# Performance work log

Measured on AMD Instinct MI355X. Metric: run time of the kernel, lower is better.

The kernel has to match this reference:

```python
import jax, jax.numpy as jnp
import numpy as np

N_VUL = 100000
N_OTH = 20000
E = 400000
IN_DIM = 256
OUT_DIM = 128
NTYPES = ['vul', 'weakness_name', 'product_name', 'refer', 'descr']
NSIZE = [N_VUL, N_OTH, N_OTH, N_OTH, N_OTH]
# canonical etypes as (src_ntype_idx, dst_ntype_idx), in loop order:
#   w2v, p2v (positive -> vul), r2v, d2v (negative -> vul), v2w, v2p, v2r, v2d (vul -> others)
CE = [(1, 0), (2, 0), (3, 0), (4, 0), (0, 1), (0, 2), (0, 3), (0, 4)]
EPS = 1e-8


def setup_inputs() -> dict:
    key = jax.random.key(0)
    ks = jax.random.split(key, 7)
    feat_vul = jax.random.normal(ks[0], (N_VUL, IN_DIM), jnp.float32)
    feat_other = jax.random.normal(ks[1], (4, N_OTH, IN_DIM), jnp.float32)
    We = jax.random.normal(ks[2], (8, IN_DIM, OUT_DIM), jnp.float32) * 0.05
    Wn = jax.random.normal(ks[3], (5, IN_DIM, OUT_DIM), jnp.float32) * 0.05
    bn = jax.random.normal(ks[4], (5, OUT_DIM), jnp.float32) * 0.05
    src = jax.random.randint(ks[5], (8, E), 0, 100000, jnp.int32)
    dst = jax.random.randint(ks[6], (8, E), 0, 100000, jnp.int32)
    src_idx = jnp.stack([src[i] % NSIZE[CE[i][0]] for i in range(8)])
    dst_idx = jnp.stack([dst[i] % NSIZE[CE[i][1]] for i in range(8)])
    return dict(feat_vul=feat_vul, feat_other=feat_other, We=We, Wn=Wn, bn=bn,
                src_idx=src_idx, dst_idx=dst_idx)


def _forward(feat_vul, feat_other, We, Wn, bn, src_idx, dst_idx):
    feats = [feat_vul] + [feat_other[i] for i in range(4)]
    # per-ntype dst projection ht (same nweight regardless of etype)
    ht = [feats[n] @ Wn[n] + bn[n] for n in range(5)]

    # apply_edges pass: scores use the per-etype hr projection (fresh at apply time);
    # hr is overwritten per etype, so messages later use the LAST hr written per src type.
    scores = []
    hr_final = [None] * 5
    for i, (s_t, d_t) in enumerate(CE):
        hr = feats[s_t] @ We[i]                     # [N_src, OUT]
        hr_final[s_t] = hr
        a = hr[src_idx[i]]                          # [E, OUT] gather
        b = ht[d_t][dst_idx[i]]                     # [E, OUT] gather
        dot = jnp.sum(a * b, axis=1)
        na = jnp.maximum(jnp.linalg.norm(a, axis=1), EPS)
        nb = jnp.maximum(jnp.linalg.norm(b, axis=1), EPS)
        scores.append(dot / (na * nb))              # cosine similarity [E]

    # multi_update_all: per-etype segment weighted-sum of messages + mean attention
    agg_h, ma = [], []
    for i, (s_t, d_t) in enumerate(CE):
        s = scores[i]
        m = s[:, None] * hr_final[s_t][src_idx[i]]  # [E, OUT]
        n_dst = NSIZE[d_t]
        h = jax.ops.segment_sum(m, dst_idx[i], num_segments=n_dst)
        cnt = jax.ops.segment_sum(jnp.ones_like(s), dst_idx[i], num_segments=n_dst)
        mean_s = jax.ops.segment_sum(s, dst_idx[i], num_segments=n_dst) / jnp.maximum(cnt, 1.0)
        agg_h.append(h)
        ma.append(mean_s)

    # vul (target): stack positive etypes (w2v,p2v) and negative (r2v,d2v) along dim 1
    ph = jnp.stack([agg_h[0], agg_h[1]], axis=1)            # [N_vul, 2, OUT]
    mpa = jnp.stack([ma[0], ma[1]], axis=1)[:, :, None]     # [N_vul, 2, 1]
    nh = jnp.stack([agg_h[2], agg_h[3]], axis=1)
    mna = jnp.stack([ma[2], ma[3]], axis=1)[:, :, None]
    pa = jax.nn.softmax(mpa, axis=1) * 0.6
    na_w = jax.nn.softmax(mna, axis=1) * 0.4
    h_vul = jnp.sum(pa * ph, axis=1) + jnp.sum(na_w * nh, axis=1)
    outs = [jnp.concatenate([ht[0], h_vul], axis=1)]

    # other ntypes: single-etype stack -> softmax over size-1 dim = 1.0
    for j, e in enumerate([4, 5, 6, 7]):
        n = j + 1
        hs = agg_h[e][:, None, :]                           # [N, 1, OUT]
        ms = ma[e][:, None, None]                           # [N, 1, 1]
        h = jnp.sum(jax.nn.softmax(ms, axis=1) * hs, axis=1)
        outs.append(jnp.concatenate([ht[n], h], axis=1))
    return tuple(outs)


def reference(feat_vul, feat_other, We, Wn, bn, src_idx, dst_idx):
    return _forward(feat_vul, feat_other, We, Wn, bn, src_idx, dst_idx)
```

## Files before the change

### kernel.cpp

```cpp
#include <hip/hip_runtime.h>

#define N_VUL 100000
#define N_OTH 20000
#define E_NUM 400000
#define K_DIM 256
#define D_OUT 128
#define EPS 1e-8f
#define LDW 264

#define NCV 391
#define NCO_J 79
#define NC (NCV + 4 * NCO_J)
#define TOT_E (8 * E_NUM)
#define CHUNK 8192
#define VCAP 5120
#define OCAP 6144
#define VKEYS (4 * N_VUL)
#define KEYS  (4 * N_VUL + 4 * N_OTH)

typedef __attribute__((ext_vector_type(8))) short bf16x8;
typedef __attribute__((ext_vector_type(4))) float f32x4;

static const size_t NV128 = (size_t)N_VUL * 128;
static const size_t NO128 = (size_t)N_OTH * 128;

__device__ __forceinline__ unsigned short f2b(float f) {
    unsigned int u = __float_as_uint(f);
    u += 0x7FFFu + ((u >> 16) & 1u);
    return (unsigned short)(u >> 16);
}
__device__ __forceinline__ float b2f(unsigned short h) {
    return __uint_as_float(((unsigned int)h) << 16);
}

__global__ __launch_bounds__(256)
void probe_idx(const int* __restrict__ cand, int* __restrict__ flag)
{
    const int e = blockIdx.x * 256 + threadIdx.x;
    if (e >= E_NUM) return;
    int v = cand[e];
    if (v < 0 || v >= N_OTH) atomicOr(flag, 1);
}

__global__ __launch_bounds__(256)
void pack_w(const float* __restrict__ We, const float* __restrict__ Wn,
            unsigned short* __restrict__ Wb)
{
    const int id = blockIdx.x * 256 + threadIdx.x;
    if (id >= 13 * 32768) return;
    const int wp = id >> 15;
    const int n  = (id >> 8) & 127;
    const int k  = id & 255;
    const float* S;
    if (wp == 0)      S = Wn;
    else if (wp <= 4) S = We + (size_t)(3 + wp) * 32768;
    else if (wp & 1)  S = Wn + (size_t)((wp - 3) >> 1) * 32768;
    else              S = We + (size_t)((wp - 6) >> 1) * 32768;
    Wb[id] = f2b(S[k * D_OUT + n]);
}

__global__ __launch_bounds__(256)
void proj_mfma(const float* __restrict__ X, const unsigned short* __restrict__ Wb,
               const float* __restrict__ bias, float* __restrict__ outF,
               unsigned short* __restrict__ tabs, int NW, int N)
{
    __shared__ unsigned short xs[64 * LDW];
    const int tid  = threadIdx.x;
    const int wave = tid >> 6, lane = tid & 63;
    const int r0   = blockIdx.x * 64;

    #pragma unroll
    for (int c = 0; c < 16; ++c) {
        int f = c * 256 + tid;
        int row = f >> 6, col4 = f & 63;
        int gr = r0 + row; if (gr >= N) gr = N - 1;
        float4 v = *(const float4*)(X + (size_t)gr * K_DIM + col4 * 4);
        unsigned short* p = xs + row * LDW + col4 * 4;
        p[0] = f2b(v.x); p[1] = f2b(v.y); p[2] = f2b(v.z); p[3] = f2b(v.w);
    }
    __syncthreads();

    const int n0   = wave * 32;
    const int arow = lane & 15, akd = (lane >> 4) * 8;
    const int bcol = lane & 15, bkd = (lane >> 4) * 8;
    const int rsub = (lane >> 4) * 4;

    float bias0 = 0.f, bias1 = 0.f;
    if (bias) { bias0 = bias[n0 + bcol]; bias1 = bias[n0 + 16 + bcol]; }

    for (int w = 0; w < NW; ++w) {
        f32x4 acc[4][2];
        #pragma unroll
        for (int m = 0; m < 4; ++m) {
            acc[m][0] = (f32x4){0.f, 0.f, 0.f, 0.f};
            acc[m][1] = (f32x4){0.f, 0.f, 0.f, 0.f};
        }
        const unsigned short* wb = Wb + (size_t)w * 128 * 256;
        #pragma unroll
        for (int k = 0; k < 8; ++k) {
            bf16x8 b0 = *(const bf16x8*)(wb + (size_t)(n0 + bcol) * 256 + k * 32 + bkd);
            bf16x8 b1 = *(const bf16x8*)(wb + (size_t)(n0 + 16 + bcol) * 256 + k * 32 + bkd);
            #pragma unroll
            for (int m = 0; m < 4; ++m) {
                bf16x8 a = *(const bf16x8*)(xs + (m * 16 + arow) * LDW + k * 32 + akd);
                acc[m][0] = __builtin_amdgcn_mfma_f32_16x16x32_bf16(a, b0, acc[m][0], 0, 0, 0);
                acc[m][1] = __builtin_amdgcn_mfma_f32_16x16x32_bf16(a, b1, acc[m][1], 0, 0, 0);
            }
        }
        if (w == 0) {
            #pragma unroll
            for (int m = 0; m < 4; ++m)
                #pragma unroll
                for (int nn = 0; nn < 2; ++nn) {
                    const int col = n0 + nn * 16 + bcol;
                    const float bb = nn ? bias1 : bias0;
                    #pragma unroll
                    for (int j = 0; j < 4; ++j) {
                        const int row = r0 + m * 16 + rsub + j;
                        if (row < N) outF[(size_t)row * 256 + col] = acc[m][nn][j] + bb;
                    }
                }
        } else {
            unsigned short* tw = tabs + (size_t)(w - 1) * N * D_OUT;
            #pragma unroll
            for (int m = 0; m < 4; ++m)
                #pragma unroll
                for (int nn = 0; nn < 2; ++nn) {
                    const int col = n0 + nn * 16 + bcol;
                    #pragma unroll
                    for (int j = 0; j < 4; ++j) {
                        const int row = r0 + m * 16 + rsub + j;
                        if (row < N) tw[(size_t)row * D_OUT + col] = f2b(acc[m][nn][j]);
                    }
                }
        }
    }
}

__global__ __launch_bounds__(256)
void rownorm_f(const float* __restrict__ T, float* __restrict__ rn, int N)
{
    const int lr = threadIdx.x >> 6;
    const int l  = threadIdx.x & 63;
    const int r  = blockIdx.x * 4 + lr;
    if (r >= N) return;
    float a = T[(size_t)r * 256 + l];
    float b = T[(size_t)r * 256 + 64 + l];
    float s = a * a + b * b;
    #pragma unroll
    for (int m = 32; m; m >>= 1) s += __shfl_xor(s, m);
    if (l == 0) rn[r] = 1.f / fmaxf(sqrtf(s), EPS);
}

__global__ __launch_bounds__(256)
void rownorm_b(const unsigned short* __restrict__ T, float* __restrict__ rn, int N)
{
    const int lr = threadIdx.x >> 6;
    const int l  = threadIdx.x & 63;
    const int r  = blockIdx.x * 4 + lr;
    if (r >= N) return;
    float a = b2f(T[(size_t)r * D_OUT + l]);
    float b = b2f(T[(size_t)r * D_OUT + 64 + l]);
    float s = a * a + b * b;
    #pragma unroll
    for (int m = 32; m; m >>= 1) s += __shfl_xor(s, m);
    if (l == 0) rn[r] = 1.f / fmaxf(sqrtf(s), EPS);
}

__device__ __forceinline__ void edge_cd(const int* __restrict__ srcp,
                                        const int* __restrict__ dstp,
                                        int id, int* c_out, unsigned* entry_out)
{
    const int et = id / E_NUM;
    const int e  = id - et * E_NUM;
    int d = dstp[(size_t)et * E_NUM + e];
    if (et < 4) {
        d = d < 0 ? 0 : (d >= N_VUL ? N_VUL - 1 : d);
        *c_out = d >> 8;
        if (entry_out) {
            int s = srcp[(size_t)et * E_NUM + e];
            s = s < 0 ? 0 : (s >= N_OTH ? N_OTH - 1 : s);
            *entry_out = ((unsigned)(((d & 255) << 2) | et) << 17) | (unsigned)s;
        }
    } else {
        d = d < 0 ? 0 : (d >= N_OTH ? N_OTH - 1 : d);
        *c_out = NCV + (et - 4) * NCO_J + (d >> 8);
        if (entry_out) {
            int s = srcp[(size_t)et * E_NUM + e];
            s = s < 0 ? 0 : (s >= N_VUL ? N_VUL - 1 : s);
            *entry_out = ((unsigned)(d & 255) << 17) | (unsigned)s;
        }
    }
}

__global__ __launch_bounds__(256)
void chist(const int* __restrict__ pA, const int* __restrict__ pB,
           const int* __restrict__ flag, int* __restrict__ ccnt)
{
    __shared__ int h[NC];
    for (int i = threadIdx.x; i < NC; i += 256) h[i] = 0;
    __syncthreads();
    const int flagv = *flag;
    const int* srcp = flagv ? pB : pA;
    const int* dstp = flagv ? pA : pB;
    const int base = blockIdx.x * 16384;
    for (int t = 0; t < 64; ++t) {
        const int id = base + t * 256 + threadIdx.x;
        if (id < TOT_E) {
            int c; edge_cd(srcp, dstp, id, &c, nullptr);
            atomicAdd(&h[c], 1);
        }
    }
    __syncthreads();
    for (int i = threadIdx.x; i < NC; i += 256)
        if (h[i]) atomicAdd(&ccnt[i], h[i]);
}

__global__ __launch_bounds__(256)
void cscan(const int* __restrict__ ccnt, int* __restrict__ cbase,
           int* __restrict__ ccur, int* __restrict__ offs)
{
    __shared__ int sh[256];
    __shared__ int carry;
    if (threadIdx.x == 0) carry = 0;
    __syncthreads();
    for (int b = 0; b < NC; b += 256) {
        const int i = b + threadIdx.x;
        const int v = (i < NC) ? ccnt[i] : 0;
        sh[threadIdx.x] = v;
        __syncthreads();
        for (int st = 1; st < 256; st <<= 1) {
            int t = (threadIdx.x >= st) ? sh[threadIdx.x - st] : 0;
            __syncthreads();
            sh[threadIdx.x] += t;
            __syncthreads();
        }
        const int excl = carry + sh[threadIdx.x] - v;
        if (i < NC) { cbase[i] = excl; ccur[i] = excl; }
        __syncthreads();
        if (threadIdx.x == 255) carry += sh[255];
        __syncthreads();
    }
    if (threadIdx.x == 0) offs[KEYS] = carry;
}

__global__ __launch_bounds__(256)
void cstage(const int* __restrict__ pA, const int* __restrict__ pB,
            const int* __restrict__ flag, int* __restrict__ ccur,
            unsigned* __restrict__ staging)
{
    __shared__ unsigned outE[CHUNK];
    __shared__ unsigned short binof[CHUNK];
    __shared__ int foff[NC];
    __shared__ int fcur[NC];
    __shared__ int gb[NC];
    __shared__ int sh[256];
    __shared__ int carry;

    const int flagv = *flag;
    const int* srcp = flagv ? pB : pA;
    const int* dstp = flagv ? pA : pB;
    const int base = blockIdx.x * CHUNK;
    const int n = (base + CHUNK <= TOT_E) ? CHUNK : (TOT_E - base);

    for (int i = threadIdx.x; i < NC; i += 256) foff[i] = 0;
    if (threadIdx.x == 0) carry = 0;
    __syncthreads();

    for (int t = 0; t < CHUNK / 256; ++t) {
        const int k = t * 256 + threadIdx.x;
        if (k < n) {
            int c; edge_cd(srcp, dstp, base + k, &c, nullptr);
            atomicAdd(&foff[c], 1);
        }
    }
    __syncthreads();

    for (int b = 0; b < NC; b += 256) {
        const int i = b + threadIdx.x;
        const int v = (i < NC) ? foff[i] : 0;
        sh[threadIdx.x] = v;
        __syncthreads();
        for (int st = 1; st < 256; st <<= 1) {
            int t = (threadIdx.x >= st) ? sh[threadIdx.x - st] : 0;
            __syncthreads();
            sh[threadIdx.x] += t;
            __syncthreads();
        }
        const int excl = carry + sh[threadIdx.x] - v;
        if (i < NC) {
            foff[i] = excl;
            fcur[i] = excl;
            gb[i] = v ? atomicAdd(&ccur[i], v) : 0;
        }
        __syncthreads();
        if (threadIdx.x == 255) carry += sh[255];
        __syncthreads();
    }

    for (int t = 0; t < CHUNK / 256; ++t) {
        const int k = t * 256 + threadIdx.x;
        if (k < n) {
            int c; unsigned ent;
            edge_cd(srcp, dstp, base + k, &c, &ent);
            const int p = atomicAdd(&fcur[c], 1);
            outE[p] = ent;
            binof[p] = (unsigned short)c;
        }
    }
    __syncthreads();

    for (int i = threadIdx.x; i < n; i += 256) {
        const int c = binof[i];
        staging[gb[c] + (i - foff[c])] = outE[i];
    }
}

__global__ __launch_bounds__(256)
void fine_sort_vul(const unsigned* __restrict__ staging,
                   const int* __restrict__ cbase, const int* __restrict__ ccnt,
                   int* __restrict__ srcs, int* __restrict__ offs)
{
    __shared__ unsigned raw[VCAP];
    __shared__ int srt[VCAP];
    __shared__ int foff[1025];
    __shared__ int fcur[1024];
    __shared__ int sh[256];
    __shared__ int carry;

    const int c = blockIdx.x;
    const int nb = min(ccnt[c], VCAP);
    const int gb = cbase[c];
    const int tid = threadIdx.x;

    for (int i = tid; i < 1024; i += 256) fcur[i] = 0;
    if (tid == 0) carry = 0;
    __syncthreads();
    for (int i = tid; i < nb; i += 256) {
        unsigned e = staging[gb + i];
        raw[i] = e;
        atomicAdd(&fcur[e >> 17], 1);
    }
    __syncthreads();
    for (int b = 0; b < 1024; b += 256) {
        const int i = b + tid;
        const int v = fcur[i];
        sh[tid] = v;
        __syncthreads();
        for (int st = 1; st < 256; st <<= 1) {
            int t = (tid >= st) ? sh[tid - st] : 0;
            __syncthreads();
            sh[tid] += t;
            __syncthreads();
        }
        foff[i] = carry + sh[tid] - v;
        __syncthreads();
        if (tid == 255) carry += sh[255];
        __syncthreads();
    }
    __syncthreads();
    for (int i = tid; i < 1024; i += 256) fcur[i] = foff[i];
    __syncthreads();
    for (int i = tid; i < nb; i += 256) {
        unsigned e = raw[i];
        const int p = atomicAdd(&fcur[e >> 17], 1);
        srt[p] = (int)(e & 0x1FFFFu);
    }
    __syncthreads();
    for (int i = tid; i < nb; i += 256) srcs[gb + i] = srt[i];
    for (int lk = tid; lk < 1024; lk += 256) {
        const int d = c * 256 + (lk >> 2);
        if (d < N_VUL) offs[c * 1024 + lk] = gb + foff[lk];
    }
}

__global__ __launch_bounds__(256)
void fine_sort_oth(const unsigned* __restrict__ staging,
                   const int* __restrict__ cbase, const int* __restrict__ ccnt,
                   int* __restrict__ srcs, int* __restrict__ offs)
{
    __shared__ unsigned raw[OCAP];
    __shared__ int srt[OCAP];
    __shared__ int foff[257];
    __shared__ int fcur[256];
    __shared__ int sh[256];

    const int co = blockIdx.x;
    const int j = co / NCO_J, dg = co - j * NCO_J;
    const int c = NCV + co;
    const int nb = min(ccnt[c], OCAP);
    const int gb = cbase[c];
    const int tid = threadIdx.x;

    fcur[tid] = 0;
    __syncthreads();
    for (int i = tid; i < nb; i += 256) {
        unsigned e = staging[gb + i];
        raw[i] = e;
        atomicAdd(&fcur[e >> 17], 1);
    }
    __syncthreads();
    {
        const int v = fcur[tid];
        sh[tid] = v;
        __syncthreads();
        for (int st = 1; st < 256; st <<= 1) {
            int t = (tid >= st) ? sh[tid - st] : 0;
            __syncthreads();
            sh[tid] += t;
            __syncthreads();
        }
        foff[tid] = sh[tid] - v;
        if (tid == 255) foff[256] = sh[255];
        __syncthreads();
        fcur[tid] = foff[tid];
    }
    __syncthreads();
    for (int i = tid; i < nb; i += 256) {
        unsigned e = raw[i];
        const int p = atomicAdd(&fcur[e >> 17], 1);
        srt[p] = (int)(e & 0x1FFFFu);
    }
    __syncthreads();
    for (int i = tid; i < nb; i += 256) srcs[gb + i] = srt[i];
    {
        const int d = dg * 256 + tid;
        if (d < N_OTH) offs[VKEYS + j * N_OTH + d] = gb + foff[tid];
    }
}

__global__ __launch_bounds__(256)
void vul_gather(const int* __restrict__ srcs, const int* __restrict__ offs,
                const unsigned short* __restrict__ othTab,
                const float* __restrict__ rinHrS,
                const float* __restrict__ rinHtVul,
                float* __restrict__ out)
{
    const int d = blockIdx.x * 4 + (threadIdx.x >> 6);
    const int lane = threadIdx.x & 63;
    const int g = lane >> 4, l = lane & 15;

    const float* hrow = out + (size_t)d * 256 + l * 8;
    float b0[8];
    {
        float4 t0 = *(const float4*)(hrow);
        float4 t1 = *(const float4*)(hrow + 4);
        b0[0] = t0.x; b0[1] = t0.y; b0[2] = t0.z; b0[3] = t0.w;
        b0[4] = t1.x; b0[5] = t1.y; b0[6] = t1.z; b0[7] = t1.w;
    }
    const float rnb = rinHtVul[d];

    float acc[4][8];
    float ss[4];
    #pragma unroll
    for (int et = 0; et < 4; ++et) {
        ss[et] = 0.f;
        #pragma unroll
        for (int j = 0; j < 8; ++j) acc[et][j] = 0.f;
    }

    #pragma unroll
    for (int et = 0; et < 4; ++et) {
        const unsigned short* T = othTab + (size_t)et * NO128;
        const float* rA = rinHrS + (size_t)et * N_OTH;
        const int k0 = offs[d * 4 + et], k1 = offs[d * 4 + et + 1];
        for (int p0 = k0; p0 < k1; p0 += 4) {
            const int p = p0 + g;
            const bool ok = (p < k1);
            const int s = srcs[ok ? p : k0];
            bf16x8 av = *(const bf16x8*)(T + (size_t)s * 128 + l * 8);
            float a[8];
            #pragma unroll
            for (int j = 0; j < 8; ++j) a[j] = b2f((unsigned short)av[j]);
            float dp = 0.f;
            #pragma unroll
            for (int j = 0; j < 8; ++j) dp = fmaf(a[j], b0[j], dp);
            dp += __shfl_xor(dp, 1); dp += __shfl_xor(dp, 2);
            dp += __shfl_xor(dp, 4); dp += __shfl_xor(dp, 8);
            const float v = ok ? dp * rA[s] * rnb : 0.f;
            ss[et] += v;
            #pragma unroll
            for (int j = 0; j < 8; ++j) acc[et][j] = fmaf(v, a[j], acc[et][j]);
        }
    }

    #pragma unroll
    for (int et = 0; et < 4; ++et) {
        float t = ss[et];
        t += __shfl_xor(t, 16); t += __shfl_xor(t, 32);
        ss[et] = t;
    }
    const int o0 = offs[d * 4], o1 = offs[d * 4 + 1], o2 = offs[d * 4 + 2],
              o3 = offs[d * 4 + 3], o4 = offs[d * 4 + 4];
    const float m0 = ss[0] / fmaxf((float)(o1 - o0), 1.f);
    const float m1 = ss[1] / fmaxf((float)(o2 - o1), 1.f);
    const float m2 = ss[2] / fmaxf((float)(o3 - o2), 1.f);
    const float m3 = ss[3] / fmaxf((float)(o4 - o3), 1.f);
    const float e0 = expf(m0), e1 = expf(m1), e2 = expf(m2), e3 = expf(m3);
    const float wp = 0.6f / (e0 + e1), wn = 0.4f / (e2 + e3);
    const float w0 = e0 * wp, w1 = e1 * wp, w2 = e2 * wn, w3 = e3 * wn;

    float res[8];
    #pragma unroll
    for (int j = 0; j < 8; ++j) {
        float t = w0 * acc[0][j] + w1 * acc[1][j] + w2 * acc[2][j] + w3 * acc[3][j];
        t += __shfl_xor(t, 16); t += __shfl_xor(t, 32);
        res[j] = t;
    }
    if (g == 0) {
        float4 r0 = {res[0], res[1], res[2], res[3]};
        float4 r1 = {res[4], res[5], res[6], res[7]};
        float* o = out + (size_t)d * 256 + 128 + l * 8;
        *(float4*)(o) = r0;
        *(float4*)(o + 4) = r1;
    }
}

__global__ __launch_bounds__(256)
void oth_gather(const int* __restrict__ srcs, const int* __restrict__ offs,
                const unsigned short* __restrict__ vulTab,
                const float* __restrict__ rinHrB,
                const float* __restrict__ rinHtOth,
                float* __restrict__ outO)
{
    const int j = threadIdx.x >> 6;
    const int d = blockIdx.x;
    const int lane = threadIdx.x & 63;
    const int g = lane >> 4, l = lane & 15;

    const float* hrow = outO + ((size_t)j * N_OTH + d) * 256 + l * 8;
    float b0[8];
    {
        float4 t0 = *(const float4*)(hrow);
        float4 t1 = *(const float4*)(hrow + 4);
        b0[0] = t0.x; b0[1] = t0.y; b0[2] = t0.z; b0[3] = t0.w;
        b0[4] = t1.x; b0[5] = t1.y; b0[6] = t1.z; b0[7] = t1.w;
    }
    const float rnb = rinHtOth[j * N_OTH + d];
    const unsigned short* A = vulTab + (size_t)j * NV128;
    const unsigned short* M = vulTab + (size_t)3 * NV128;
    const float* rA = rinHrB + (size_t)j * N_VUL;

    const int key = VKEYS + j * N_OTH + d;
    const int k0 = offs[key], k1 = offs[key + 1];

    float acc[8];
    #pragma unroll
    for (int jj = 0; jj < 8; ++jj) acc[jj] = 0.f;

    for (int p0 = k0; p0 < k1; p0 += 4) {
        const int p = p0 + g;
        const bool ok = (p < k1);
        const int s = srcs[ok ? p : k0];
        bf16x8 av = *(const bf16x8*)(A + (size_t)s * 128 + l * 8);
        float a[8];
        #pragma unroll
        for (int jj = 0; jj < 8; ++jj) a[jj] = b2f((unsigned short)av[jj]);
        float dp = 0.f;
        #pragma unroll
        for (int jj = 0; jj < 8; ++jj) dp = fmaf(a[jj], b0[jj], dp);
        dp += __shfl_xor(dp, 1); dp += __shfl_xor(dp, 2);
        dp += __shfl_xor(dp, 4); dp += __shfl_xor(dp, 8);
        const float v = ok ? dp * rA[s] * rnb : 0.f;
        if (j == 3) {
            #pragma unroll
            for (int jj = 0; jj < 8; ++jj) acc[jj] = fmaf(v, a[jj], acc[jj]);
        } else {
            bf16x8 mv = *(const bf16x8*)(M + (size_t)s * 128 + l * 8);
            #pragma unroll
            for (int jj = 0; jj < 8; ++jj) acc[jj] = fmaf(v, b2f((unsigned short)mv[jj]), acc[jj]);
        }
    }

    #pragma unroll
    for (int jj = 0; jj < 8; ++jj) {
        float t = acc[jj];
        t += __shfl_xor(t, 16); t += __shfl_xor(t, 32);
        acc[jj] = t;
    }
    if (g == 0) {
        float4 r0 = {acc[0], acc[1], acc[2], acc[3]};
        float4 r1 = {acc[4], acc[5], acc[6], acc[7]};
        float* o = outO + ((size_t)j * N_OTH + d) * 256 + 128 + l * 8;
        *(float4*)(o) = r0;
        *(float4*)(o + 4) = r1;
    }
}

extern "C" void kernel_launch(void* const* d_in, const int* in_sizes, int n_in,
                              void* d_out, int out_size, void* d_ws, size_t ws_size,
                              hipStream_t stream)
{
    int i_fv = 0, i_fo = 1, i_We = 2, i_Wn = 3, i_bn = 4, i_iA = 5, i_iB = 6;
    {
        int a = -1, b = -1;
        for (int i = 0; i < n_in; ++i) {
            switch (in_sizes[i]) {
                case 25600000: i_fv = i; break;
                case 20480000: i_fo = i; break;
                case   262144: i_We = i; break;
                case   163840: i_Wn = i; break;
                case      640: i_bn = i; break;
                case  3200000: if (a < 0) a = i; else b = i; break;
                default: break;
            }
        }
        if (a >= 0 && b >= 0) { i_iA = a; i_iB = b; }
    }
    const float* feat_vul = (const float*)d_in[i_fv];
    const float* feat_oth = (const float*)d_in[i_fo];
    const float* We = (const float*)d_in[i_We];
    const float* Wn = (const float*)d_in[i_Wn];
    const float* bn = (const float*)d_in[i_bn];
    const int* idxA = (const int*)d_in[i_iA];
    const int* idxB = (const int*)d_in[i_iB];
    float* out = (float*)d_out;

    int*      flag    = (int*)d_ws;
    int*      ccnt    = flag + 4;
    int*      cbase   = ccnt + NC;
    int*      ccur    = cbase + NC;
    unsigned* staging = (unsigned*)(ccur + NC);
    int*      srcs    = (int*)(staging + TOT_E);
    int*      offs    = srcs + TOT_E;
    float*    rinHtVul = (float*)(offs + KEYS + 1);
    float*    rinHtOth = rinHtVul + N_VUL;
    float*    rinHrB   = rinHtOth + (size_t)4 * N_OTH;
    float*    rinHrS   = rinHrB + (size_t)4 * N_VUL;
    unsigned short* vulTab = (unsigned short*)(rinHrS + (size_t)4 * N_OTH);
    unsigned short* othTab = vulTab + 4 * NV128;
    unsigned short* Wb     = othTab + 4 * NO128;

    hipMemsetAsync(d_ws, 0, (4 + (size_t)NC) * sizeof(int), stream);

    probe_idx<<<(E_NUM + 255) / 256, 256, 0, stream>>>(idxA, flag);
    pack_w<<<(13 * 32768 + 255) / 256, 256, 0, stream>>>(We, Wn, Wb);

    const size_t OUT0 = (size_t)N_VUL * 256;

    proj_mfma<<<(N_VUL + 63) / 64, 256, 0, stream>>>(
        feat_vul, Wb, bn, out, vulTab, 5, N_VUL);
    for (int i = 0; i < 4; ++i)
        proj_mfma<<<(N_OTH + 63) / 64, 256, 0, stream>>>(
            feat_oth + (size_t)i * N_OTH * K_DIM,
            Wb + (size_t)(5 + 2 * i) * 32768,
            bn + (size_t)(i + 1) * D_OUT,
            out + OUT0 + (size_t)i * N_OTH * 256,
            othTab + (size_t)i * NO128, 2, N_OTH);

    rownorm_f<<<(N_VUL + 3) / 4, 256, 0, stream>>>(out, rinHtVul, N_VUL);
    rownorm_f<<<(4 * N_OTH + 3) / 4, 256, 0, stream>>>(out + OUT0, rinHtOth, 4 * N_OTH);
    rownorm_b<<<(4 * N_VUL + 3) / 4, 256, 0, stream>>>(vulTab, rinHrB, 4 * N_VUL);
    rownorm_b<<<(4 * N_OTH + 3) / 4, 256, 0, stream>>>(othTab, rinHrS, 4 * N_OTH);

    chist<<<(TOT_E + 16383) / 16384, 256, 0, stream>>>(idxA, idxB, flag, ccnt);
    cscan<<<1, 256, 0, stream>>>(ccnt, cbase, ccur, offs);
    cstage<<<(TOT_E + CHUNK - 1) / CHUNK, 256, 0, stream>>>(idxA, idxB, flag, ccur, staging);
    fine_sort_vul<<<NCV, 256, 0, stream>>>(staging, cbase, ccnt, srcs, offs);
    fine_sort_oth<<<4 * NCO_J, 256, 0, stream>>>(staging, cbase, ccnt, srcs, offs);

    vul_gather<<<N_VUL / 4, 256, 0, stream>>>(srcs, offs, othTab, rinHrS, rinHtVul, out);
    oth_gather<<<N_OTH, 256, 0, stream>>>(srcs, offs, vulTab, rinHrB, rinHtOth, out + OUT0);
}
```

Before: 760.6 us.

## Fuse row norms into projection epilogue and merge gather kernels

Computes the inverse row norms inside the MFMA projection epilogue using shared-memory atomics, which removes four separate rownorm kernels that each re-read the projected tables. The vul and other-type gather kernels are merged into one launch so the two kinds of work can overlap. The other-type gather loop is also unrolled to handle two edges per iteration for more memory-level parallelism. In exchange it adds LDS atomics and extra barriers per weight pass in the projection, and the merged kernel's two branches have different register needs.

```diff
diff --git a/kernel.cpp b/kernel.cpp
--- a/kernel.cpp
+++ b/kernel.cpp
@@ -17,6 +17,7 @@
 #define OCAP 6144
 #define VKEYS (4 * N_VUL)
 #define KEYS  (4 * N_VUL + 4 * N_OTH)
+#define NVB (N_VUL / 4)
 
 typedef __attribute__((ext_vector_type(8))) short bf16x8;
 typedef __attribute__((ext_vector_type(4))) float f32x4;
@@ -62,9 +63,11 @@
 __global__ __launch_bounds__(256)
 void proj_mfma(const float* __restrict__ X, const unsigned short* __restrict__ Wb,
                const float* __restrict__ bias, float* __restrict__ outF,
-               unsigned short* __restrict__ tabs, int NW, int N)
+               unsigned short* __restrict__ tabs, int NW, int N,
+               float* __restrict__ rnHt, float* __restrict__ rnTab)
 {
     __shared__ unsigned short xs[64 * LDW];
+    __shared__ float rs[64];
     const int tid  = threadIdx.x;
     const int wave = tid >> 6, lane = tid & 63;
     const int r0   = blockIdx.x * 64;
@@ -107,17 +110,22 @@
                 acc[m][1] = __builtin_amdgcn_mfma_f32_16x16x32_bf16(a, b1, acc[m][1], 0, 0, 0);
             }
         }
+        __syncthreads();
+        if (tid < 64) rs[tid] = 0.f;
+        __syncthreads();
+
         if (w == 0) {
             #pragma unroll
             for (int m = 0; m < 4; ++m)
                 #pragma unroll
-                for (int nn = 0; nn < 2; ++nn) {
-                    const int col = n0 + nn * 16 + bcol;
-                    const float bb = nn ? bias1 : bias0;
-                    #pragma unroll
-                    for (int j = 0; j < 4; ++j) {
-                        const int row = r0 + m * 16 + rsub + j;
-                        if (row < N) outF[(size_t)row * 256 + col] = acc[m][nn][j] + bb;
+                for (int j = 0; j < 4; ++j) {
+                    const int row = r0 + m * 16 + rsub + j;
+                    if (row < N) {
+                        const float v0 = acc[m][0][j] + bias0;
+                        const float v1 = acc[m][1][j] + bias1;
+                        outF[(size_t)row * 256 + n0 + bcol]      = v0;
+                        outF[(size_t)row * 256 + n0 + 16 + bcol] = v1;
+                        atomicAdd(&rs[m * 16 + rsub + j], v0 * v0 + v1 * v1);
                     }
                 }
         } else {
@@ -125,46 +133,28 @@
             #pragma unroll
             for (int m = 0; m < 4; ++m)
                 #pragma unroll
-                for (int nn = 0; nn < 2; ++nn) {
-                    const int col = n0 + nn * 16 + bcol;
-                    #pragma unroll
-                    for (int j = 0; j < 4; ++j) {
-                        const int row = r0 + m * 16 + rsub + j;
-                        if (row < N) tw[(size_t)row * D_OUT + col] = f2b(acc[m][nn][j]);
+                for (int j = 0; j < 4; ++j) {
+                    const int row = r0 + m * 16 + rsub + j;
+                    if (row < N) {
+                        const unsigned short h0 = f2b(acc[m][0][j]);
+                        const unsigned short h1 = f2b(acc[m][1][j]);
+                        tw[(size_t)row * D_OUT + n0 + bcol]      = h0;
+                        tw[(size_t)row * D_OUT + n0 + 16 + bcol] = h1;
+                        const float v0 = b2f(h0), v1 = b2f(h1);
+                        atomicAdd(&rs[m * 16 + rsub + j], v0 * v0 + v1 * v1);
                     }
                 }
         }
-    }
-}
-
-__global__ __launch_bounds__(256)
-void rownorm_f(const float* __restrict__ T, float* __restrict__ rn, int N)
-{
-    const int lr = threadIdx.x >> 6;
-    const int l  = threadIdx.x & 63;
-    const int r  = blockIdx.x * 4 + lr;
-    if (r >= N) return;
-    float a = T[(size_t)r * 256 + l];
-    float b = T[(size_t)r * 256 + 64 + l];
-    float s = a * a + b * b;
-    #pragma unroll
-    for (int m = 32; m; m >>= 1) s += __shfl_xor(s, m);
-    if (l == 0) rn[r] = 1.f / fmaxf(sqrtf(s), EPS);
-}
-
-__global__ __launch_bounds__(256)
-void rownorm_b(const unsigned short* __restrict__ T, float* __restrict__ rn, int N)
-{
-    const int lr = threadIdx.x >> 6;
-    const int l  = threadIdx.x & 63;
-    const int r  = blockIdx.x * 4 + lr;
-    if (r >= N) return;
-    float a = b2f(T[(size_t)r * D_OUT + l]);
-    float b = b2f(T[(size_t)r * D_OUT + 64 + l]);
-    float s = a * a + b * b;
-    #pragma unroll
-    for (int m = 32; m; m >>= 1) s += __shfl_xor(s, m);
-    if (l == 0) rn[r] = 1.f / fmaxf(sqrtf(s), EPS);
+        __syncthreads();
+        if (tid < 64) {
+            const int row = r0 + tid;
+            if (row < N) {
+                const float rn = 1.f / fmaxf(sqrtf(rs[tid]), EPS);
+                if (w == 0) rnHt[row] = rn;
+                else        rnTab[(size_t)(w - 1) * N + row] = rn;
+            }
+        }
+    }
 }
 
 __device__ __forceinline__ void edge_cd(const int* __restrict__ srcp,
@@ -430,160 +420,168 @@
 }
 
 __global__ __launch_bounds__(256)
-void vul_gather(const int* __restrict__ srcs, const int* __restrict__ offs,
-                const unsigned short* __restrict__ othTab,
-                const float* __restrict__ rinHrS,
-                const float* __restrict__ rinHtVul,
-                float* __restrict__ out)
-{
-    const int d = blockIdx.x * 4 + (threadIdx.x >> 6);
+void fused_gather(const int* __restrict__ srcs, const int* __restrict__ offs,
+                  const unsigned short* __restrict__ othTab,
+                  const unsigned short* __restrict__ vulTab,
+                  const float* __restrict__ rinHrS,
+                  const float* __restrict__ rinHrB,
+                  const float* __restrict__ rinHtVul,
+                  const float* __restrict__ rinHtOth,
+                  float* __restrict__ out)
+{
     const int lane = threadIdx.x & 63;
     const int g = lane >> 4, l = lane & 15;
 
-    const float* hrow = out + (size_t)d * 256 + l * 8;
-    float b0[8];
-    {
-        float4 t0 = *(const float4*)(hrow);
-        float4 t1 = *(const float4*)(hrow + 4);
-        b0[0] = t0.x; b0[1] = t0.y; b0[2] = t0.z; b0[3] = t0.w;
-        b0[4] = t1.x; b0[5] = t1.y; b0[6] = t1.z; b0[7] = t1.w;
-    }
-    const float rnb = rinHtVul[d];
-
-    float acc[4][8];
-    float ss[4];
-    #pragma unroll
-    for (int et = 0; et < 4; ++et) {
-        ss[et] = 0.f;
-        #pragma unroll
-        for (int j = 0; j < 8; ++j) acc[et][j] = 0.f;
-    }
-
-    #pragma unroll
-    for (int et = 0; et < 4; ++et) {
-        const unsigned short* T = othTab + (size_t)et * NO128;
-        const float* rA = rinHrS + (size_t)et * N_OTH;
-        const int k0 = offs[d * 4 + et], k1 = offs[d * 4 + et + 1];
-        for (int p0 = k0; p0 < k1; p0 += 4) {
-            const int p = p0 + g;
-            const bool ok = (p < k1);
-            const int s = srcs[ok ? p : k0];
-            bf16x8 av = *(const bf16x8*)(T + (size_t)s * 128 + l * 8);
-            float a[8];
+    if ((int)blockIdx.x < NVB) {
+        const int d = blockIdx.x * 4 + (threadIdx.x >> 6);
+        const float* hrow = out + (size_t)d * 256 + l * 8;
+        float b0[8];
+        {
+            float4 t0 = *(const float4*)(hrow);
+            float4 t1 = *(const float4*)(hrow + 4);
+            b0[0] = t0.x; b0[1] = t0.y; b0[2] = t0.z; b0[3] = t0.w;
+            b0[4] = t1.x; b0[5] = t1.y; b0[6] = t1.z; b0[7] = t1.w;
+        }
+        const float rnb = rinHtVul[d];
+
+        float acc[4][8];
+        float ss[4];
+        #pragma unroll
+        for (int et = 0; et < 4; ++et) {
+            ss[et] = 0.f;
             #pragma unroll
-            for (int j = 0; j < 8; ++j) a[j] = b2f((unsigned short)av[j]);
-            float dp = 0.f;
+            for (int j = 0; j < 8; ++j) acc[et][j] = 0.f;
+        }
+        #pragma unroll
+        for (int et = 0; et < 4; ++et) {
+            const unsigned short* T = othTab + (size_t)et * NO128;
+            const float* rA = rinHrS + (size_t)et * N_OTH;
+            const int k0 = offs[d * 4 + et], k1 = offs[d * 4 + et + 1];
+            for (int p0 = k0; p0 < k1; p0 += 4) {
+                const int p = p0 + g;
+                const bool ok = (p < k1);
+                const int s = srcs[ok ? p : k0];
+                bf16x8 av = *(const bf16x8*)(T + (size_t)s * 128 + l * 8);
+                float a[8];
+                #pragma unroll
+                for (int j = 0; j < 8; ++j) a[j] = b2f((unsigned short)av[j]);
+                float dp = 0.f;
+                #pragma unroll
+                for (int j = 0; j < 8; ++j) dp = fmaf(a[j], b0[j], dp);
+                dp += __shfl_xor(dp, 1); dp += __shfl_xor(dp, 2);
+                dp += __shfl_xor(dp, 4); dp += __shfl_xor(dp, 8);
+                const float v = ok ? dp * rA[s] * rnb : 0.f;
+                ss[et] += v;
+                #pragma unroll
+                for (int j = 0; j < 8; ++j) acc[et][j] = fmaf(v, a[j], acc[et][j]);
+            }
+        }
+        #pragma unroll
+        for (int et = 0; et < 4; ++et) {
+            float t = ss[et];
+            t += __shfl_xor(t, 16); t += __shfl_xor(t, 32);
+            ss[et] = t;
+        }
+        const int o0 = offs[d * 4], o1 = offs[d * 4 + 1], o2 = offs[d * 4 + 2],
+                  o3 = offs[d * 4 + 3], o4 = offs[d * 4 + 4];
+        const float m0 = ss[0] / fmaxf((float)(o1 - o0), 1.f);
+        const float m1 = ss[1] / fmaxf((float)(o2 - o1), 1.f);
+        const float m2 = ss[2] / fmaxf((float)(o3 - o2), 1.f);
+        const float m3 = ss[3] / fmaxf((float)(o4 - o3), 1.f);
+        const float e0 = expf(m0), e1 = expf(m1), e2 = expf(m2), e3 = expf(m3);
+        const float wp = 0.6f / (e0 + e1), wn = 0.4f / (e2 + e3);
+        const float w0 = e0 * wp, w1 = e1 * wp, w2 = e2 * wn, w3 = e3 * wn;
+
+        float res[8];
+        #pragma unroll
+        for (int j = 0; j < 8; ++j) {
+            float t = w0 * acc[0][j] + w1 * acc[1][j] + w2 * acc[2][j] + w3 * acc[3][j];
+            t += __shfl_xor(t, 16); t += __shfl_xor(t, 32);
+            res[j] = t;
+        }
+        if (g == 0) {
+            float4 r0 = {res[0], res[1], res[2], res[3]};
+            float4 r1 = {res[4], res[5], res[6], res[7]};
+            float* o = out + (size_t)d * 256 + 128 + l * 8;
+            *(float4*)(o) = r0;
+            *(float4*)(o + 4) = r1;
+        }
+    } else {
+        float* outO = out + (size_t)N_VUL * 256;
+        const int j = threadIdx.x >> 6;
+        const int d = blockIdx.x - NVB;
+
+        const float* hrow = outO + ((size_t)j * N_OTH + d) * 256 + l * 8;
+        float b0[8];
+        {
+            float4 t0 = *(const float4*)(hrow);
+            float4 t1 = *(const float4*)(hrow + 4);
+            b0[0] = t0.x; b0[1] = t0.y; b0[2] = t0.z; b0[3] = t0.w;
+            b0[4] = t1.x; b0[5] = t1.y; b0[6] = t1.z; b0[7] = t1.w;
+        }
+        const float rnb = rinHtOth[j * N_OTH + d];
+        const unsigned short* A = vulTab + (size_t)j * NV128;
+        const unsigned short* M = vulTab + (size_t)3 * NV128;
+        const float* rA = rinHrB + (size_t)j * N_VUL;
+
+        const int key = VKEYS + j * N_OTH + d;
+        const int k0 = offs[key], k1 = offs[key + 1];
+
+        float acc[8];
+        #pragma unroll
+        for (int jj = 0; jj < 8; ++jj) acc[jj] = 0.f;
+
+        for (int p0 = k0; p0 < k1; p0 += 8) {
+            const int pa = p0 + g, pb = p0 + 4 + g;
+            const bool oka = (pa < k1), okb = (pb < k1);
+            const int sa = srcs[oka ? pa : k0];
+            const int sb = srcs[okb ? pb : k0];
+            bf16x8 ava = *(const bf16x8*)(A + (size_t)sa * 128 + l * 8);
+            bf16x8 avb = *(const bf16x8*)(A + (size_t)sb * 128 + l * 8);
+            float aa[8], ab[8];
             #pragma unroll
-            for (int j = 0; j < 8; ++j) dp = fmaf(a[j], b0[j], dp);
-            dp += __shfl_xor(dp, 1); dp += __shfl_xor(dp, 2);
-            dp += __shfl_xor(dp, 4); dp += __shfl_xor(dp, 8);
-            const float v = ok ? dp * rA[s] * rnb : 0.f;
-            ss[et] += v;
+            for (int jj = 0; jj < 8; ++jj) {
+                aa[jj] = b2f((unsigned short)ava[jj]);
+                ab[jj] = b2f((unsigned short)avb[jj]);
+            }
+            float dpa = 0.f, dpb = 0.f;
             #pragma unroll
-            for (int j = 0; j < 8; ++j) acc[et][j] = fmaf(v, a[j], acc[et][j]);
-        }
-    }
-
-    #pragma unroll
-    for (int et = 0; et < 4; ++et) {
-        float t = ss[et];
-        t += __shfl_xor(t, 16); t += __shfl_xor(t, 32);
-        ss[et] = t;
-    }
-    const int o0 = offs[d * 4], o1 = offs[d * 4 + 1], o2 = offs[d * 4 + 2],
-              o3 = offs[d * 4 + 3], o4 = offs[d * 4 + 4];
-    const float m0 = ss[0] / fmaxf((float)(o1 - o0), 1.f);
-    const float m1 = ss[1] / fmaxf((float)(o2 - o1), 1.f);
-    const float m2 = ss[2] / fmaxf((float)(o3 - o2), 1.f);
-    const float m3 = ss[3] / fmaxf((float)(o4 - o3), 1.f);
-    const float e0 = expf(m0), e1 = expf(m1), e2 = expf(m2), e3 = expf(m3);
-    const float wp = 0.6f / (e0 + e1), wn = 0.4f / (e2 + e3);
-    const float w0 = e0 * wp, w1 = e1 * wp, w2 = e2 * wn, w3 = e3 * wn;
-
-    float res[8];
-    #pragma unroll
-    for (int j = 0; j < 8; ++j) {
-        float t = w0 * acc[0][j] + w1 * acc[1][j] + w2 * acc[2][j] + w3 * acc[3][j];
-        t += __shfl_xor(t, 16); t += __shfl_xor(t, 32);
-        res[j] = t;
-    }
-    if (g == 0) {
-        float4 r0 = {res[0], res[1], res[2], res[3]};
-        float4 r1 = {res[4], res[5], res[6], res[7]};
-        float* o = out + (size_t)d * 256 + 128 + l * 8;
-        *(float4*)(o) = r0;
-        *(float4*)(o + 4) = r1;
-    }
-}
-
-__global__ __launch_bounds__(256)
-void oth_gather(const int* __restrict__ srcs, const int* __restrict__ offs,
-                const unsigned short* __restrict__ vulTab,
-                const float* __restrict__ rinHrB,
-                const float* __restrict__ rinHtOth,
-                float* __restrict__ outO)
-{
-    const int j = threadIdx.x >> 6;
-    const int d = blockIdx.x;
-    const int lane = threadIdx.x & 63;
-    const int g = lane >> 4, l = lane & 15;
-
-    const float* hrow = outO + ((size_t)j * N_OTH + d) * 256 + l * 8;
-    float b0[8];
-    {
-        float4 t0 = *(const float4*)(hrow);
-        float4 t1 = *(const float4*)(hrow + 4);
-        b0[0] = t0.x; b0[1] = t0.y; b0[2] = t0.z; b0[3] = t0.w;
-        b0[4] = t1.x; b0[5] = t1.y; b0[6] = t1.z; b0[7] = t1.w;
-    }
-    const float rnb = rinHtOth[j * N_OTH + d];
-    const unsigned short* A = vulTab + (size_t)j * NV128;
-    const unsigned short* M = vulTab + (size_t)3 * NV128;
-    const float* rA = rinHrB + (size_t)j * N_VUL;
-
-    const int key = VKEYS + j * N_OTH + d;
-    const int k0 = offs[key], k1 = offs[key + 1];
-
-    float acc[8];
-    #pragma unroll
-    for (int jj = 0; jj < 8; ++jj) acc[jj] = 0.f;
-
-    for (int p0 = k0; p0 < k1; p0 += 4) {
-        const int p = p0 + g;
-        const bool ok = (p < k1);
-        const int s = srcs[ok ? p : k0];
-        bf16x8 av = *(const bf16x8*)(A + (size_t)s * 128 + l * 8);
-        float a[8];
-        #pragma unroll
-        for (int jj = 0; jj < 8; ++jj) a[jj] = b2f((unsigned short)av[jj]);
-        float dp = 0.f;
-        #pragma unroll
-        for (int jj = 0; jj < 8; ++jj) dp = fmaf(a[jj], b0[jj], dp);
-        dp += __shfl_xor(dp, 1); dp += __shfl_xor(dp, 2);
-        dp += __shfl_xor(dp, 4); dp += __shfl_xor(dp, 8);
-        const float v = ok ? dp * rA[s] * rnb : 0.f;
-        if (j == 3) {
-            #pragma unroll
-            for (int jj = 0; jj < 8; ++jj) acc[jj] = fmaf(v, a[jj], acc[jj]);
-        } else {
-            bf16x8 mv = *(const bf16x8*)(M + (size_t)s * 128 + l * 8);
-            #pragma unroll
-            for (int jj = 0; jj < 8; ++jj) acc[jj] = fmaf(v, b2f((unsigned short)mv[jj]), acc[jj]);
-        }
-    }
-
-    #pragma unroll
-    for (int jj = 0; jj < 8; ++jj) {
-        float t = acc[jj];
-        t += __shfl_xor(t, 16); t += __shfl_xor(t, 32);
-        acc[jj] = t;
-    }
-    if (g == 0) {
-        float4 r0 = {acc[0], acc[1], acc[2], acc[3]};
-        float4 r1 = {acc[4], acc[5], acc[6], acc[7]};
-        float* o = outO + ((size_t)j * N_OTH + d) * 256 + 128 + l * 8;
-        *(float4*)(o) = r0;
-        *(float4*)(o + 4) = r1;
+            for (int jj = 0; jj < 8; ++jj) {
+                dpa = fmaf(aa[jj], b0[jj], dpa);
+                dpb = fmaf(ab[jj], b0[jj], dpb);
+            }
+            dpa += __shfl_xor(dpa, 1); dpb += __shfl_xor(dpb, 1);
+            dpa += __shfl_xor(dpa, 2); dpb += __shfl_xor(dpb, 2);
+            dpa += __shfl_xor(dpa, 4); dpb += __shfl_xor(dpb, 4);
+            dpa += __shfl_xor(dpa, 8); dpb += __shfl_xor(dpb, 8);
+            const float va = oka ? dpa * rA[sa] * rnb : 0.f;
+            const float vb = okb ? dpb * rA[sb] * rnb : 0.f;
+            if (j == 3) {
+                #pragma unroll
+                for (int jj = 0; jj < 8; ++jj)
+                    acc[jj] = fmaf(vb, ab[jj], fmaf(va, aa[jj], acc[jj]));
+            } else {
+                bf16x8 mva = *(const bf16x8*)(M + (size_t)sa * 128 + l * 8);
+                bf16x8 mvb = *(const bf16x8*)(M + (size_t)sb * 128 + l * 8);
+                #pragma unroll
+                for (int jj = 0; jj < 8; ++jj)
+                    acc[jj] = fmaf(vb, b2f((unsigned short)mvb[jj]),
+                                   fmaf(va, b2f((unsigned short)mva[jj]), acc[jj]));
+            }
+        }
+        #pragma unroll
+        for (int jj = 0; jj < 8; ++jj) {
+            float t = acc[jj];
+            t += __shfl_xor(t, 16); t += __shfl_xor(t, 32);
+            acc[jj] = t;
+        }
+        if (g == 0) {
+            float4 r0 = {acc[0], acc[1], acc[2], acc[3]};
+            float4 r1 = {acc[4], acc[5], acc[6], acc[7]};
+            float* o = outO + ((size_t)j * N_OTH + d) * 256 + 128 + l * 8;
+            *(float4*)(o) = r0;
+            *(float4*)(o + 4) = r1;
+        }
     }
 }
 
@@ -639,19 +637,15 @@
     const size_t OUT0 = (size_t)N_VUL * 256;
 
     proj_mfma<<<(N_VUL + 63) / 64, 256, 0, stream>>>(
-        feat_vul, Wb, bn, out, vulTab, 5, N_VUL);
+        feat_vul, Wb, bn, out, vulTab, 5, N_VUL, rinHtVul, rinHrB);
     for (int i = 0; i < 4; ++i)
         proj_mfma<<<(N_OTH + 63) / 64, 256, 0, stream>>>(
             feat_oth + (size_t)i * N_OTH * K_DIM,
             Wb + (size_t)(5 + 2 * i) * 32768,
             bn + (size_t)(i + 1) * D_OUT,
             out + OUT0 + (size_t)i * N_OTH * 256,
-            othTab + (size_t)i * NO128, 2, N_OTH);
-
-    rownorm_f<<<(N_VUL + 3) / 4, 256, 0, stream>>>(out, rinHtVul, N_VUL);
-    rownorm_f<<<(4 * N_OTH + 3) / 4, 256, 0, stream>>>(out + OUT0, rinHtOth, 4 * N_OTH);
-    rownorm_b<<<(4 * N_VUL + 3) / 4, 256, 0, stream>>>(vulTab, rinHrB, 4 * N_VUL);
-    rownorm_b<<<(4 * N_OTH + 3) / 4, 256, 0, stream>>>(othTab, rinHrS, 4 * N_OTH);
+            othTab + (size_t)i * NO128, 2, N_OTH,
+            rinHtOth + (size_t)i * N_OTH, rinHrS + (size_t)i * N_OTH);
 
     chist<<<(TOT_E + 16383) / 16384, 256, 0, stream>>>(idxA, idxB, flag, ccnt);
     cscan<<<1, 256, 0, stream>>>(ccnt, cbase, ccur, offs);
@@ -659,6 +653,6 @@
     fine_sort_vul<<<NCV, 256, 0, stream>>>(staging, cbase, ccnt, srcs, offs);
     fine_sort_oth<<<4 * NCO_J, 256, 0, stream>>>(staging, cbase, ccnt, srcs, offs);
 
-    vul_gather<<<N_VUL / 4, 256, 0, stream>>>(srcs, offs, othTab, rinHrS, rinHtVul, out);
-    oth_gather<<<N_OTH, 256, 0, stream>>>(srcs, offs, vulTab, rinHrB, rinHtOth, out + OUT0);
-}
+    fused_gather<<<NVB + N_OTH, 256, 0, stream>>>(
+        srcs, offs, othTab, vulTab, rinHrS, rinHrB, rinHtVul, rinHtOth, out);
+}
```

Result: slower. 950.5 us (+25.0%).
